# Optimization experiments

Measured on AMD Instinct MI355X. Metric: run time of the kernel, lower is better.

Reference implementation:

```python
import jax, jax.numpy as jnp
import numpy as np

B, A, C, H, W = 2, 4, 3, 32, 32
N = H * W * A  # 4096 proposals
EPS = 1e-6


def setup_inputs() -> dict:
    key = jax.random.key(0)
    k1, k2, k3, k4 = jax.random.split(key, 4)
    scores = jax.random.normal(k1, (B, A * C, H, W), jnp.float32)
    bbox_preds = jax.random.normal(k2, (B, A * 7, H, W), jnp.float32)
    pp_params = jax.random.normal(k3, (B, C * 3, H, W), jnp.float32)
    # decoded LiDAR boxes (x, y, z, dx, dy, dz, yaw) with positive sizes
    u = jax.random.uniform(k4, (B, N, 7), jnp.float32)
    scale = jnp.array([80.0, 80.0, 4.0, 4.0, 4.0, 3.0, 6.28], jnp.float32)
    shift = jnp.array([-40.0, -40.0, -2.0, 0.5, 0.5, 0.5, -3.14], jnp.float32)
    decoded = u * scale + shift
    return {"scores": scores, "bbox_preds": bbox_preds,
            "pp_params": pp_params, "decoded": decoded}


def _nearest_bev(dec):
    # dec: [B, N, 7] -> axis-aligned nearest BEV boxes [B, N, 4] (x1,y1,x2,y2)
    bev = dec[..., jnp.array([0, 1, 3, 4, 6])]  # x, y, dx, dy, yaw
    rot = bev[..., 4]
    period = jnp.pi
    # limit_period(rot, offset=0.5, period=pi)
    normed = jnp.abs(rot - jnp.floor(rot / period + 0.5) * period)
    cond = (normed > jnp.pi / 4)[..., None]
    xywh = jnp.where(cond, bev[..., jnp.array([0, 1, 3, 2])], bev[..., :4])
    ctr, dims = xywh[..., :2], xywh[..., 2:]
    return jnp.concatenate([ctr - dims / 2, ctr + dims / 2], axis=-1)


def _pairwise_iou(boxes):
    # boxes: [B, N, 4] -> iou [B, N, N]
    lt = jnp.maximum(boxes[:, :, None, :2], boxes[:, None, :, :2])
    rb = jnp.minimum(boxes[:, :, None, 2:], boxes[:, None, :, 2:])
    wh = jnp.clip(rb - lt, 0.0)
    inter = wh[..., 0] * wh[..., 1]
    area = (boxes[..., 2] - boxes[..., 0]) * (boxes[..., 3] - boxes[..., 1])
    union = area[:, :, None] + area[:, None, :] - inter
    return inter / jnp.maximum(union, EPS)


def _forward_scores(scores, pp_params, decoded):
    # flatten scores: [B, A*C, H, W] -> [B, N, C]
    sc = scores.reshape(B, A, C, H, W).transpose(0, 3, 4, 1, 2).reshape(B, N, C)
    # flatten pp: [B, C*3, H, W] -> [B, H, W, C, 3] -> expand over A -> [B, N, C, 3]
    pp = pp_params.reshape(B, C, 3, H, W).transpose(0, 3, 4, 1, 2)
    pp = jnp.broadcast_to(pp[:, :, :, None], (B, H, W, A, C, 3)).reshape(B, N, C, 3)

    iou = _pairwise_iou(_nearest_bev(decoded[..., :7]))  # [B, N, N]
    sm_sc = jax.nn.softmax(sc, axis=1)  # softmax over proposal dim per class

    per_class = []
    for c in range(C):  # C is small and fixed
        p0 = pp[:, :, c, 0]
        p1 = pp[:, :, c, 1]
        weight = jax.nn.softmax(iou + p0[:, :, None] * p1[:, None, :], axis=2)
        per_class.append(jnp.einsum('bij,bj->bi', weight, sm_sc[:, :, c]))
    new_sc = jnp.stack(per_class, axis=-1)  # [B, N, C]

    # back to level layout: [B, N, C] -> [B, A*C, H, W]
    return new_sc.reshape(B, H, W, A, C).transpose(0, 3, 4, 1, 2).reshape(B, A * C, H, W)


def reference(scores, bbox_preds, pp_params, decoded):
    out_scores = _forward_scores(scores, pp_params, decoded)
    # original returns (out_scores_list, bbox_preds, dir_cls, pp_params); dir_cls=None
    return out_scores, bbox_preds, pp_params
```

## Files before the change

kernel.cpp:

```cpp
#include <hip/hip_runtime.h>
#include <math.h>

#define B_   2
#define C_   3
#define HW_  1024
#define N_   4096
#define AC_  12
#define JSPLIT 16
#define JTILE  256
#define ROWBLK 128
#define PI_F 3.14159265358979323846f
#define L2E     1.4426950408889634f
#define INV_L2E 0.6931471805599453f

#define OUT0_ELEMS 24576
#define OUT1_ELEMS 57344
#define OUT2_ELEMS 18432

#define WS_JBOX  0
#define WS_JAUX  32768
#define WS_JP1   65536
#define WS_JP0   98304
#define WS_PART  131072
#define WS_STATS 917504

#if __has_builtin(__builtin_amdgcn_exp2f)
#define EXP2F(x) __builtin_amdgcn_exp2f(x)
#else
#define EXP2F(x) __expf((x) * INV_L2E)
#endif

#define PREP_JBLKS 16
#define PREP_CPBLKS 80
#define CP_F4_BBOX 14336
#define CP_F4_TOT  18944

__device__ __forceinline__ float4 make_box(const float* __restrict__ d) {
    float x = d[0], y = d[1], d3 = d[3], d4 = d[4], rot = d[6];
    float kq = floorf(rot / PI_F + 0.5f);
    float normed = fabsf(rot - kq * PI_F);
    bool swap_wh = normed > (0.25f * PI_F);
    float w = swap_wh ? d4 : d3;
    float h = swap_wh ? d3 : d4;
    return make_float4(x - 0.5f * w, y - 0.5f * h, x + 0.5f * w, y + 0.5f * h);
}

__global__ __launch_bounds__(256) void k_prep(
    const float* __restrict__ scores, const float* __restrict__ pp,
    const float* __restrict__ dec, const float* __restrict__ bbox,
    float* __restrict__ ws, float* __restrict__ out)
{
    const int blk = blockIdx.x;
    const int t = threadIdx.x;

    if (blk >= PREP_JBLKS) {
        const float4* src1 = (const float4*)bbox;
        const float4* src2 = (const float4*)pp;
        float4* dst1 = (float4*)(out + OUT0_ELEMS);
        float4* dst2 = (float4*)(out + OUT0_ELEMS + OUT1_ELEMS);
        for (int u = (blk - PREP_JBLKS) * 256 + t; u < CP_F4_TOT;
             u += PREP_CPBLKS * 256) {
            if (u < CP_F4_BBOX) dst1[u] = src1[u];
            else                dst2[u - CP_F4_BBOX] = src2[u - CP_F4_BBOX];
        }
        return;
    }

    const int b = blk >> 3, seg = blk & 7;
    const float* decb = dec + b * N_ * 7;
    float4* jbox = (float4*)(ws + WS_JBOX) + b * N_;
    float4* jaux = (float4*)(ws + WS_JAUX) + b * N_;
    float4* jp1  = (float4*)(ws + WS_JP1)  + b * N_;
    float4* jp0  = (float4*)(ws + WS_JP0)  + b * N_;

    __shared__ float red[4][3];
    float ls0 = 0.f, ls1 = 0.f, ls2 = 0.f;
    const int n0 = seg * 512;
    for (int n = n0 + t; n < n0 + 512; n += 256) {
        const int hw = n >> 2, a = n & 3;
        float4 box = make_box(decb + n * 7);
        float area = (box.z - box.x) * (box.w - box.y);
        float e0 = __expf(scores[(b * AC_ + a * C_ + 0) * HW_ + hw]);
        float e1 = __expf(scores[(b * AC_ + a * C_ + 1) * HW_ + hw]);
        float e2 = __expf(scores[(b * AC_ + a * C_ + 2) * HW_ + hw]);
        ls0 += e0; ls1 += e1; ls2 += e2;
        jbox[n] = box;
        jaux[n] = make_float4(area * INV_L2E, e0, e1, e2);
        jp1[n]  = make_float4(pp[(b * 9 + 1) * HW_ + hw],
                              pp[(b * 9 + 4) * HW_ + hw],
                              pp[(b * 9 + 7) * HW_ + hw], 0.f);
        jp0[n]  = make_float4(pp[(b * 9 + 0) * HW_ + hw] * L2E,
                              pp[(b * 9 + 3) * HW_ + hw] * L2E,
                              pp[(b * 9 + 6) * HW_ + hw] * L2E, 0.f);
    }
#pragma unroll
    for (int off = 1; off < 64; off <<= 1) {
        ls0 += __shfl_xor(ls0, off);
        ls1 += __shfl_xor(ls1, off);
        ls2 += __shfl_xor(ls2, off);
    }
    if ((t & 63) == 0) { red[t >> 6][0] = ls0; red[t >> 6][1] = ls1; red[t >> 6][2] = ls2; }
    __syncthreads();
    if (t < 3)
        ws[WS_STATS + (b * C_ + t) * 8 + seg] =
            red[0][t] + red[1][t] + red[2][t] + red[3][t];
}

__global__ __launch_bounds__(256) void k_main(float* __restrict__ ws)
{
    const int b = blockIdx.y;
    const int jb = blockIdx.x & 15;
    const int rowblk = blockIdx.x >> 4;
    const int t = threadIdx.x;
    const int q = t >> 6;
    const int r = t & 63;

    const float4* jbox = (const float4*)(ws + WS_JBOX) + b * N_;
    const float4* jaux = (const float4*)(ws + WS_JAUX) + b * N_;
    const float4* jp1  = (const float4*)(ws + WS_JP1)  + b * N_;
    const float4* jp0  = (const float4*)(ws + WS_JP0)  + b * N_;

    __shared__ float4 s_box[JTILE];
    __shared__ float4 s_aux[JTILE];
    __shared__ float4 s_p1[JTILE];
    __shared__ float2 s_m[C_][ROWBLK][4];

    const int jbase = jb * JTILE;
    s_box[t] = jbox[jbase + t];
    s_aux[t] = jaux[jbase + t];
    s_p1[t]  = jp1[jbase + t];

    const int i0 = rowblk * ROWBLK + r, i1 = i0 + 64;
    const float4 bx0 = jbox[i0], bx1 = jbox[i1];
    const float  ar0 = jaux[i0].x, ar1 = jaux[i1].x;
    const float4 p0v0 = jp0[i0], p0v1 = jp0[i1];

    __syncthreads();

    float n00 = 0.f, d00 = 0.f, n01 = 0.f, d01 = 0.f, n02 = 0.f, d02 = 0.f;
    float n10 = 0.f, d10 = 0.f, n11 = 0.f, d11 = 0.f, n12 = 0.f, d12 = 0.f;

#pragma unroll 4
    for (int jj = q; jj < JTILE; jj += 4) {
        const float4 bj = s_box[jj];
        const float4 ax = s_aux[jj];
        const float4 pj = s_p1[jj];
        {
            float x1 = fmaxf(bx0.x, bj.x), y1 = fmaxf(bx0.y, bj.y);
            float x2 = fminf(bx0.z, bj.z), y2 = fminf(bx0.w, bj.w);
            float w = fmaxf(x2 - x1, 0.f), h = fmaxf(y2 - y1, 0.f);
            float inter = w * h;
            float uni = fmaf(inter, -INV_L2E, ar0 + ax.x);
            float iou = inter * __builtin_amdgcn_rcpf(uni);
            float e0 = EXP2F(fmaf(p0v0.x, pj.x, iou));
            float e1 = EXP2F(fmaf(p0v0.y, pj.y, iou));
            float e2 = EXP2F(fmaf(p0v0.z, pj.z, iou));
            n00 = fmaf(e0, ax.y, n00); d00 += e0;
            n01 = fmaf(e1, ax.z, n01); d01 += e1;
            n02 = fmaf(e2, ax.w, n02); d02 += e2;
        }
        {
            float x1 = fmaxf(bx1.x, bj.x), y1 = fmaxf(bx1.y, bj.y);
            float x2 = fminf(bx1.z, bj.z), y2 = fminf(bx1.w, bj.w);
            float w = fmaxf(x2 - x1, 0.f), h = fmaxf(y2 - y1, 0.f);
            float inter = w * h;
            float uni = fmaf(inter, -INV_L2E, ar1 + ax.x);
            float iou = inter * __builtin_amdgcn_rcpf(uni);
            float e0 = EXP2F(fmaf(p0v1.x, pj.x, iou));
            float e1 = EXP2F(fmaf(p0v1.y, pj.y, iou));
            float e2 = EXP2F(fmaf(p0v1.z, pj.z, iou));
            n10 = fmaf(e0, ax.y, n10); d10 += e0;
            n11 = fmaf(e1, ax.z, n11); d11 += e1;
            n12 = fmaf(e2, ax.w, n12); d12 += e2;
        }
    }

    s_m[0][r][q] = make_float2(n00, d00);
    s_m[1][r][q] = make_float2(n01, d01);
    s_m[2][r][q] = make_float2(n02, d02);
    s_m[0][r + 64][q] = make_float2(n10, d10);
    s_m[1][r + 64][q] = make_float2(n11, d11);
    s_m[2][r + 64][q] = make_float2(n12, d12);
    __syncthreads();

    float2* part = (float2*)(ws + WS_PART);
    for (int u = t; u < C_ * ROWBLK; u += 256) {
        const int c = u >> 7, row = u & 127;
        float2 a0 = s_m[c][row][0], a1 = s_m[c][row][1];
        float2 a2 = s_m[c][row][2], a3 = s_m[c][row][3];
        part[((b * JSPLIT + jb) * C_ + c) * N_ + rowblk * ROWBLK + row] =
            make_float2(a0.x + a1.x + a2.x + a3.x, a0.y + a1.y + a2.y + a3.y);
    }
}

__global__ __launch_bounds__(256) void k_reduce(
    const float* __restrict__ ws, float* __restrict__ out)
{
    const int tid = blockIdx.x * 256 + threadIdx.x;
    const int bc = tid >> 12;
    const int i  = tid & 4095;
    const int b = bc / C_, c = bc % C_;
    const float2* part = (const float2*)(ws + WS_PART);
    float num = 0.f, den = 0.f;
#pragma unroll
    for (int jb = 0; jb < JSPLIT; ++jb) {
        float2 v = part[((b * JSPLIT + jb) * C_ + c) * N_ + i];
        num += v.x; den += v.y;
    }
    float S = 0.f;
#pragma unroll
    for (int s = 0; s < 8; ++s) S += ws[WS_STATS + bc * 8 + s];
    out[(b * AC_ + (i & 3) * 3 + c) * HW_ + (i >> 2)] = num / (den * S);
}

extern "C" void kernel_launch(void* const* d_in, const int* in_sizes, int n_in,
                              void* d_out, int out_size, void* d_ws, size_t ws_size,
                              hipStream_t stream) {
    const float* scores = (const float*)d_in[0];
    const float* bbox   = (const float*)d_in[1];
    const float* pp     = (const float*)d_in[2];
    const float* dec    = (const float*)d_in[3];
    float* out = (float*)d_out;
    float* ws  = (float*)d_ws;

    k_prep<<<PREP_JBLKS + PREP_CPBLKS, 256, 0, stream>>>(scores, pp, dec, bbox, ws, out);
    k_main<<<dim3(32 * JSPLIT, B_), 256, 0, stream>>>(ws);
    k_reduce<<<OUT0_ELEMS / 256, 256, 0, stream>>>(ws, out);
}
```

Baseline: 93.40 us.

## Fuse prep kernel into main and recompute softmax sums in reduce

Removes the separate prep kernel. Each main block now builds its own column tile (boxes, exp scores, pp params) and its row-side boxes straight from the raw inputs, and the passthrough copies run in extra blocks of the same grid. The per-class softmax denominators are recomputed inside each reduce block instead of being read from a precomputed stats buffer. This cuts one launch and the workspace round trip, at the cost of redundant box and exp computation across blocks.

```diff
diff --git a/kernel.cpp b/kernel.cpp
--- a/kernel.cpp
+++ b/kernel.cpp
@@ -9,6 +9,8 @@
 #define JSPLIT 16
 #define JTILE  256
 #define ROWBLK 128
+#define MAINBLKS 512
+#define CPBLKS   40
 #define PI_F 3.14159265358979323846f
 #define L2E     1.4426950408889634f
 #define INV_L2E 0.6931471805599453f
@@ -17,23 +19,17 @@
 #define OUT1_ELEMS 57344
 #define OUT2_ELEMS 18432
 
-#define WS_JBOX  0
-#define WS_JAUX  32768
-#define WS_JP1   65536
-#define WS_JP0   98304
-#define WS_PART  131072
-#define WS_STATS 917504
+#define CP_F4_BBOX 14336
+#define CP_F4_TOT  18944
+#define CP_F4_HALF 9472
+
+#define WS_PART  0
 
 #if __has_builtin(__builtin_amdgcn_exp2f)
 #define EXP2F(x) __builtin_amdgcn_exp2f(x)
 #else
 #define EXP2F(x) __expf((x) * INV_L2E)
 #endif
-
-#define PREP_JBLKS 16
-#define PREP_CPBLKS 80
-#define CP_F4_BBOX 14336
-#define CP_F4_TOT  18944
 
 __device__ __forceinline__ float4 make_box(const float* __restrict__ d) {
     float x = d[0], y = d[1], d3 = d[3], d4 = d[4], rot = d[6];
@@ -45,95 +41,65 @@
     return make_float4(x - 0.5f * w, y - 0.5f * h, x + 0.5f * w, y + 0.5f * h);
 }
 
-__global__ __launch_bounds__(256) void k_prep(
+__global__ __launch_bounds__(256) void k_main(
     const float* __restrict__ scores, const float* __restrict__ pp,
     const float* __restrict__ dec, const float* __restrict__ bbox,
     float* __restrict__ ws, float* __restrict__ out)
 {
-    const int blk = blockIdx.x;
+    const int b = blockIdx.y;
+    const int bx = blockIdx.x;
     const int t = threadIdx.x;
 
-    if (blk >= PREP_JBLKS) {
-        const float4* src1 = (const float4*)bbox;
-        const float4* src2 = (const float4*)pp;
-        float4* dst1 = (float4*)(out + OUT0_ELEMS);
-        float4* dst2 = (float4*)(out + OUT0_ELEMS + OUT1_ELEMS);
-        for (int u = (blk - PREP_JBLKS) * 256 + t; u < CP_F4_TOT;
-             u += PREP_CPBLKS * 256) {
-            if (u < CP_F4_BBOX) dst1[u] = src1[u];
-            else                dst2[u - CP_F4_BBOX] = src2[u - CP_F4_BBOX];
+    if (bx >= MAINBLKS) {
+        const int u = (bx - MAINBLKS) * 256 + t;
+        if (u < CP_F4_HALF) {
+            const int g = b * CP_F4_HALF + u;
+            if (g < CP_F4_BBOX)
+                ((float4*)(out + OUT0_ELEMS))[g] = ((const float4*)bbox)[g];
+            else
+                ((float4*)(out + OUT0_ELEMS + OUT1_ELEMS))[g - CP_F4_BBOX] =
+                    ((const float4*)pp)[g - CP_F4_BBOX];
         }
         return;
     }
 
-    const int b = blk >> 3, seg = blk & 7;
+    const int jb = bx & 15, rowblk = bx >> 4;
+    const int q = t >> 6;
+    const int r = t & 63;
     const float* decb = dec + b * N_ * 7;
-    float4* jbox = (float4*)(ws + WS_JBOX) + b * N_;
-    float4* jaux = (float4*)(ws + WS_JAUX) + b * N_;
-    float4* jp1  = (float4*)(ws + WS_JP1)  + b * N_;
-    float4* jp0  = (float4*)(ws + WS_JP0)  + b * N_;
-
-    __shared__ float red[4][3];
-    float ls0 = 0.f, ls1 = 0.f, ls2 = 0.f;
-    const int n0 = seg * 512;
-    for (int n = n0 + t; n < n0 + 512; n += 256) {
-        const int hw = n >> 2, a = n & 3;
-        float4 box = make_box(decb + n * 7);
+
+    __shared__ float4 s_box[JTILE];
+    __shared__ float4 s_aux[JTILE];
+    __shared__ float4 s_p1[JTILE];
+    __shared__ float2 s_m[C_][ROWBLK][4];
+
+    {
+        const int j = jb * JTILE + t;
+        const int hw = j >> 2, a = j & 3;
+        float4 box = make_box(decb + j * 7);
         float area = (box.z - box.x) * (box.w - box.y);
         float e0 = __expf(scores[(b * AC_ + a * C_ + 0) * HW_ + hw]);
         float e1 = __expf(scores[(b * AC_ + a * C_ + 1) * HW_ + hw]);
         float e2 = __expf(scores[(b * AC_ + a * C_ + 2) * HW_ + hw]);
-        ls0 += e0; ls1 += e1; ls2 += e2;
-        jbox[n] = box;
-        jaux[n] = make_float4(area * INV_L2E, e0, e1, e2);
-        jp1[n]  = make_float4(pp[(b * 9 + 1) * HW_ + hw],
-                              pp[(b * 9 + 4) * HW_ + hw],
-                              pp[(b * 9 + 7) * HW_ + hw], 0.f);
-        jp0[n]  = make_float4(pp[(b * 9 + 0) * HW_ + hw] * L2E,
-                              pp[(b * 9 + 3) * HW_ + hw] * L2E,
-                              pp[(b * 9 + 6) * HW_ + hw] * L2E, 0.f);
-    }
-#pragma unroll
-    for (int off = 1; off < 64; off <<= 1) {
-        ls0 += __shfl_xor(ls0, off);
-        ls1 += __shfl_xor(ls1, off);
-        ls2 += __shfl_xor(ls2, off);
-    }
-    if ((t & 63) == 0) { red[t >> 6][0] = ls0; red[t >> 6][1] = ls1; red[t >> 6][2] = ls2; }
-    __syncthreads();
-    if (t < 3)
-        ws[WS_STATS + (b * C_ + t) * 8 + seg] =
-            red[0][t] + red[1][t] + red[2][t] + red[3][t];
-}
-
-__global__ __launch_bounds__(256) void k_main(float* __restrict__ ws)
-{
-    const int b = blockIdx.y;
-    const int jb = blockIdx.x & 15;
-    const int rowblk = blockIdx.x >> 4;
-    const int t = threadIdx.x;
-    const int q = t >> 6;
-    const int r = t & 63;
-
-    const float4* jbox = (const float4*)(ws + WS_JBOX) + b * N_;
-    const float4* jaux = (const float4*)(ws + WS_JAUX) + b * N_;
-    const float4* jp1  = (const float4*)(ws + WS_JP1)  + b * N_;
-    const float4* jp0  = (const float4*)(ws + WS_JP0)  + b * N_;
-
-    __shared__ float4 s_box[JTILE];
-    __shared__ float4 s_aux[JTILE];
-    __shared__ float4 s_p1[JTILE];
-    __shared__ float2 s_m[C_][ROWBLK][4];
-
-    const int jbase = jb * JTILE;
-    s_box[t] = jbox[jbase + t];
-    s_aux[t] = jaux[jbase + t];
-    s_p1[t]  = jp1[jbase + t];
+        s_box[t] = box;
+        s_aux[t] = make_float4(area * INV_L2E, e0, e1, e2);
+        s_p1[t]  = make_float4(pp[(b * 9 + 1) * HW_ + hw],
+                               pp[(b * 9 + 4) * HW_ + hw],
+                               pp[(b * 9 + 7) * HW_ + hw], 0.f);
+    }
 
     const int i0 = rowblk * ROWBLK + r, i1 = i0 + 64;
-    const float4 bx0 = jbox[i0], bx1 = jbox[i1];
-    const float  ar0 = jaux[i0].x, ar1 = jaux[i1].x;
-    const float4 p0v0 = jp0[i0], p0v1 = jp0[i1];
+    const float4 bx0 = make_box(decb + i0 * 7);
+    const float4 bx1 = make_box(decb + i1 * 7);
+    const float ar0 = (bx0.z - bx0.x) * (bx0.w - bx0.y) * INV_L2E;
+    const float ar1 = (bx1.z - bx1.x) * (bx1.w - bx1.y) * INV_L2E;
+    const int hw0 = i0 >> 2, hw1 = i1 >> 2;
+    const float4 p0v0 = make_float4(pp[(b * 9 + 0) * HW_ + hw0] * L2E,
+                                    pp[(b * 9 + 3) * HW_ + hw0] * L2E,
+                                    pp[(b * 9 + 6) * HW_ + hw0] * L2E, 0.f);
+    const float4 p0v1 = make_float4(pp[(b * 9 + 0) * HW_ + hw1] * L2E,
+                                    pp[(b * 9 + 3) * HW_ + hw1] * L2E,
+                                    pp[(b * 9 + 6) * HW_ + hw1] * L2E, 0.f);
 
     __syncthreads();
 
@@ -194,12 +160,26 @@
 }
 
 __global__ __launch_bounds__(256) void k_reduce(
-    const float* __restrict__ ws, float* __restrict__ out)
+    const float* __restrict__ scores, const float* __restrict__ ws,
+    float* __restrict__ out)
 {
-    const int tid = blockIdx.x * 256 + threadIdx.x;
+    const int t = threadIdx.x;
+    const int tid = blockIdx.x * 256 + t;
     const int bc = tid >> 12;
     const int i  = tid & 4095;
     const int b = bc / C_, c = bc % C_;
+
+    __shared__ float red[4];
+    const float* scb = scores + (b * AC_ + c) * HW_;
+    float ls = 0.f;
+    for (int n = t; n < N_; n += 256)
+        ls += __expf(scb[(n & 3) * 3 * HW_ + (n >> 2)]);
+#pragma unroll
+    for (int off = 1; off < 64; off <<= 1) ls += __shfl_xor(ls, off);
+    if ((t & 63) == 0) red[t >> 6] = ls;
+    __syncthreads();
+    const float S = red[0] + red[1] + red[2] + red[3];
+
     const float2* part = (const float2*)(ws + WS_PART);
     float num = 0.f, den = 0.f;
 #pragma unroll
@@ -207,9 +187,6 @@
         float2 v = part[((b * JSPLIT + jb) * C_ + c) * N_ + i];
         num += v.x; den += v.y;
     }
-    float S = 0.f;
-#pragma unroll
-    for (int s = 0; s < 8; ++s) S += ws[WS_STATS + bc * 8 + s];
     out[(b * AC_ + (i & 3) * 3 + c) * HW_ + (i >> 2)] = num / (den * S);
 }
 
@@ -223,7 +200,6 @@
     float* out = (float*)d_out;
     float* ws  = (float*)d_ws;
 
-    k_prep<<<PREP_JBLKS + PREP_CPBLKS, 256, 0, stream>>>(scores, pp, dec, bbox, ws, out);
-    k_main<<<dim3(32 * JSPLIT, B_), 256, 0, stream>>>(ws);
-    k_reduce<<<OUT0_ELEMS / 256, 256, 0, stream>>>(ws, out);
-}
+    k_main<<<dim3(MAINBLKS + CPBLKS, B_), 256, 0, stream>>>(scores, pp, dec, bbox, ws, out);
+    k_reduce<<<OUT0_ELEMS / 256, 256, 0, stream>>>(scores, ws, out);
+}
```

Result: slower. 95.79 us (+2.5%).
